# Kernel optimization log

Measured on AMD Instinct MI355X. Metric: run time of the kernel, lower is better.

## Reference

```python
import jax, jax.numpy as jnp
import numpy as np
from jax.scipy.special import logsumexp


def _lstm(x, mask, Wk, Wr, b, reverse=False):
    # x: [B,T,D], mask: [B,T] bool. Keras LSTM defaults: gate order i,f,g,o,
    # sigmoid recurrent activation, tanh activation. Masked steps carry state.
    if reverse:
        x = x[:, ::-1]
        mask = mask[:, ::-1]
    B, T, _ = x.shape
    H = Wr.shape[0]
    xz = jnp.einsum('btd,dh->bth', x, Wk) + b  # [B,T,4H] input projections, done once

    def step(carry, inp):
        h, c = carry
        z_t, m = inp  # [B,4H], [B]
        z = z_t + h @ Wr
        i, f, g, o = jnp.split(z, 4, axis=-1)
        i = jax.nn.sigmoid(i)
        f = jax.nn.sigmoid(f)
        g = jnp.tanh(g)
        o = jax.nn.sigmoid(o)
        c_new = f * c + i * g
        h_new = o * jnp.tanh(c_new)
        m = m[:, None]
        h = jnp.where(m, h_new, h)
        c = jnp.where(m, c_new, c)
        return (h, c), h

    h0 = jnp.zeros((B, H), x.dtype)
    (_, _), hs = jax.lax.scan(step, (h0, h0), (xz.transpose(1, 0, 2), mask.T))
    hs = hs.transpose(1, 0, 2)  # [B,T,H]
    if reverse:
        hs = hs[:, ::-1]
    return hs


def _crf_log_likelihood(logits, tags, lengths, trans):
    # TFA crf_log_likelihood: sequence_score - log_norm (forward algorithm)
    B, T, C = logits.shape
    t_idx = jnp.arange(T)
    mask = t_idx[None, :] < lengths[:, None]  # [B,T]
    # unary score: sum_t logits[b,t,tags[b,t]] over valid t
    unary = jnp.take_along_axis(logits, tags[..., None], axis=2)[..., 0]
    unary = jnp.sum(jnp.where(mask, unary, 0.0), axis=1)
    # binary score: sum_t trans[tags[t], tags[t+1]] for t < len-1
    binary = trans[tags[:, :-1], tags[:, 1:]]  # [B,T-1]
    mask2 = t_idx[None, : T - 1] < (lengths - 1)[:, None]
    binary = jnp.sum(jnp.where(mask2, binary, 0.0), axis=1)
    # log normalizer via forward algorithm scan
    alpha0 = logits[:, 0]  # [B,C]

    def step(alpha, inp):
        logit_t, m = inp  # [B,C], [B]
        new = logsumexp(alpha[:, :, None] + trans[None], axis=1) + logit_t
        alpha = jnp.where(m[:, None], new, alpha)
        return alpha, None

    alpha, _ = jax.lax.scan(step, alpha0,
                            (logits[:, 1:].transpose(1, 0, 2), mask[:, 1:].T))
    log_norm = logsumexp(alpha, axis=1)
    return unary + binary - log_norm


def setup_inputs() -> dict:
    key = jax.random.key(0)
    ks = jax.random.split(key, 12)
    V, D, H, C, B, T = 30000, 300, 256, 9, 64, 512
    lengths = jax.random.randint(ks[0], (B,), T // 4, T + 1).astype(jnp.int32)
    valid = jnp.arange(T)[None, :] < lengths[:, None]
    inputs = (jax.random.randint(ks[1], (B, T), 1, V) * valid).astype(jnp.int32)
    targets = (jax.random.randint(ks[2], (B, T), 0, C) * valid).astype(jnp.int32)
    s = 0.05
    return {
        'inputs': inputs,
        'inputs_length': lengths,
        'targets': targets,
        'embedding': jax.random.normal(ks[3], (V, D), jnp.float32) * s,
        'Wk_f': jax.random.normal(ks[4], (D, 4 * H), jnp.float32) * s,
        'Wr_f': jax.random.normal(ks[5], (H, 4 * H), jnp.float32) * s,
        'b_f': jnp.zeros((4 * H,), jnp.float32),
        'Wk_b': jax.random.normal(ks[6], (D, 4 * H), jnp.float32) * s,
        'Wr_b': jax.random.normal(ks[7], (H, 4 * H), jnp.float32) * s,
        'b_b': jnp.zeros((4 * H,), jnp.float32),
        'dense_W': jax.random.normal(ks[8], (2 * H, C), jnp.float32) * s,
        'dense_b': jnp.zeros((C,), jnp.float32),
        'trans': jax.random.uniform(ks[9], (C, C), jnp.float32),
    }


def reference(inputs, inputs_length, targets, embedding, Wk_f, Wr_f, b_f,
              Wk_b, Wr_b, b_b, dense_W, dense_b, trans):
    T = inputs.shape[1]
    mask = jnp.arange(T)[None, :] < inputs_length[:, None]  # [B,T]
    emb = embedding[inputs]  # [B,T,D] (dropout is identity in inference)
    h_f = _lstm(emb, mask, Wk_f, Wr_f, b_f, reverse=False)
    h_b = _lstm(emb, mask, Wk_b, Wr_b, b_b, reverse=True)
    h = jnp.concatenate([h_f, h_b], axis=-1)  # [B,T,2H]
    logits = h @ dense_W + dense_b  # [B,T,C]
    log_likelihood = _crf_log_likelihood(logits, targets, inputs_length, trans)
    return logits, log_likelihood, trans
```

## Files before the change

kernel.cpp:

```cpp
#include <hip/hip_runtime.h>
#include <cstdint>
#include <cstddef>

typedef unsigned int  u32;
typedef unsigned short u16;
typedef _Float16 f16;
typedef _Float16 f16x2 __attribute__((ext_vector_type(2)));
typedef _Float16 half8 __attribute__((ext_vector_type(8)));
typedef float    f32x4v __attribute__((ext_vector_type(4)));
typedef int      i32x4 __attribute__((ext_vector_type(4)));

#define BATCH 64
#define TSEQ  512
#define DEMB  300
#define KPAD  320
#define HDIM  256
#define G4    1024
#define NCLS  9

__device__ __forceinline__ u32 packf16(float a, float b) {
  f16x2 v; v.x = (f16)a; v.y = (f16)b;
  return __builtin_bit_cast(u32, v);
}
__device__ __forceinline__ float f16f(u16 x) {
  return (float)__builtin_bit_cast(f16, x);
}
__device__ __forceinline__ float sigm_fast(float x) {
  return __builtin_amdgcn_rcpf(1.f + __expf(-x));
}
__device__ __forceinline__ float tanh_fast(float x) {
  float ax = __builtin_fabsf(x);
  float e = __expf(-2.f * ax);
  float t = (1.f - e) * __builtin_amdgcn_rcpf(1.f + e);
  return copysignf(t, x);
}

__global__ __launch_bounds__(256) void embcvt_k(const float* __restrict__ emb,
                                                u16* __restrict__ out) {
  const int v  = blockIdx.x * 16 + (threadIdx.x >> 4);
  const int kc = threadIdx.x & 15;
  u32* __restrict__ dst = (u32*)(out + (size_t)v * KPAD + kc * 20);
  if (kc < 15) {
    const float* __restrict__ src = emb + (size_t)v * DEMB + kc * 20;
    float tmp[20];
#pragma unroll
    for (int j = 0; j < 20; ++j) tmp[j] = src[j];
#pragma unroll
    for (int j = 0; j < 10; ++j) dst[j] = packf16(tmp[2 * j], tmp[2 * j + 1]);
  } else {
#pragma unroll
    for (int j = 0; j < 10; ++j) dst[j] = 0u;
  }
}

__global__ __launch_bounds__(256) void wkt_k(const float* __restrict__ Wk_f,
                                             const float* __restrict__ Wk_b,
                                             u16* __restrict__ wkt) {
  const int dir = blockIdx.y;
  const float* __restrict__ Wk = dir ? Wk_b : Wk_f;
  const int col = blockIdx.x * 16 + (threadIdx.x >> 4);
  const int kc  = threadIdx.x & 15;
  u32* __restrict__ dst = (u32*)(wkt + ((size_t)dir * G4 + col) * KPAD + kc * 20);
  if (kc < 15) {
    float tmp[20];
#pragma unroll
    for (int j = 0; j < 20; ++j) tmp[j] = Wk[(size_t)(kc * 20 + j) * G4 + col];
#pragma unroll
    for (int j = 0; j < 10; ++j) dst[j] = packf16(tmp[2 * j], tmp[2 * j + 1]);
  } else {
#pragma unroll
    for (int j = 0; j < 10; ++j) dst[j] = 0u;
  }
}

__global__ __launch_bounds__(256) void wr8_k(const float* __restrict__ Wr_f,
                                             const float* __restrict__ Wr_b,
                                             signed char* __restrict__ wr8) {
  const int dir = blockIdx.y;
  const float* __restrict__ Wr = dir ? Wr_b : Wr_f;
  const int col = blockIdx.x * 16 + (threadIdx.x >> 4);
  const int k0  = (threadIdx.x & 15) * 16;
  float tmp[16];
#pragma unroll
  for (int j = 0; j < 16; ++j) tmp[j] = Wr[(size_t)(k0 + j) * G4 + col];
  u32 pw[4];
#pragma unroll
  for (int jj = 0; jj < 4; ++jj) {
    u32 p = 0;
#pragma unroll
    for (int b = 0; b < 4; ++b) {
      int q = (int)__builtin_rintf(tmp[4 * jj + b] * 512.f);
      q = q > 127 ? 127 : (q < -127 ? -127 : q);
      p |= ((u32)(q & 255)) << (8 * b);
    }
    pw[jj] = p;
  }
  *(uint4*)(wr8 + ((size_t)dir * G4 + col) * HDIM + k0) =
      make_uint4(pw[0], pw[1], pw[2], pw[3]);
}

__global__ __launch_bounds__(256) void xz_gemm_k(
    const int* __restrict__ inputs, const u16* __restrict__ wkt,
    const u16* __restrict__ embf16, const float* __restrict__ b_f,
    const float* __restrict__ b_b, u16* __restrict__ xz)
{
  __shared__ __align__(16) u16 As[128 * 40];
  __shared__ __align__(16) u16 Bs[128 * 40];
  const int tid  = threadIdx.x;
  const int wv   = tid >> 6, lane = tid & 63;
  const int quad = lane >> 4, fl = lane & 15;
  const int cbi  = blockIdx.x;
  const int dir  = cbi >> 3;
  const int cb1  = (cbi & 7) * 128;
  const int rb   = blockIdx.y * 128;
  const float* __restrict__ bias = dir ? b_b : b_f;

  const int sm = tid >> 1, sh = (tid & 1) * 16;
  const int vrow = inputs[rb + sm];
  const u16* __restrict__ asrc = wkt + ((size_t)(dir * G4) + cb1 + sm) * KPAD + sh;
  const u16* __restrict__ bsrc = embf16 + (size_t)vrow * KPAD + sh;

  f32x4v acc[2][8];
#pragma unroll
  for (int bt = 0; bt < 2; ++bt)
#pragma unroll
    for (int i = 0; i < 8; ++i) acc[bt][i] = (f32x4v){0.f, 0.f, 0.f, 0.f};

  for (int kt = 0; kt < 10; ++kt) {
    const int k0 = kt * 32;
    uint4 a0v = *(const uint4*)(asrc + k0);
    uint4 a1v = *(const uint4*)(asrc + k0 + 8);
    uint4 b0v = *(const uint4*)(bsrc + k0);
    uint4 b1v = *(const uint4*)(bsrc + k0 + 8);
    *(uint4*)&As[sm * 40 + sh]     = a0v;
    *(uint4*)&As[sm * 40 + sh + 8] = a1v;
    *(uint4*)&Bs[sm * 40 + sh]     = b0v;
    *(uint4*)&Bs[sm * 40 + sh + 8] = b1v;
    __syncthreads();
    half8 bf[2];
#pragma unroll
    for (int bt = 0; bt < 2; ++bt)
      bf[bt] = *(const half8*)&Bs[(wv * 32 + bt * 16 + fl) * 40 + quad * 8];
#pragma unroll
    for (int i = 0; i < 8; ++i) {
      half8 af = *(const half8*)&As[(i * 16 + fl) * 40 + quad * 8];
      acc[0][i] = __builtin_amdgcn_mfma_f32_16x16x32_f16(af, bf[0], acc[0][i], 0, 0, 0);
      acc[1][i] = __builtin_amdgcn_mfma_f32_16x16x32_f16(af, bf[1], acc[1][i], 0, 0, 0);
    }
    __syncthreads();
  }
#pragma unroll
  for (int bt = 0; bt < 2; ++bt) {
    const int row = rb + wv * 32 + bt * 16 + fl;
    u16* __restrict__ orow = xz + ((size_t)(dir * BATCH * TSEQ) + row) * G4;
#pragma unroll
    for (int i = 0; i < 8; ++i) {
      const int mb = cb1 + i * 16 + quad * 4;
      const float4 bb = *(const float4*)&bias[mb];
      f32x4v v = acc[bt][i];
      uint2 pk;
      pk.x = packf16(v[0] + bb.x, v[1] + bb.y);
      pk.y = packf16(v[2] + bb.z, v[3] + bb.w);
      *(uint2*)&orow[mb] = pk;
    }
  }
}

#define MFI(a, b, c) __builtin_amdgcn_mfma_i32_16x16x64_i8(a, b, c, 0, 0, 0)
#define LD8(g, ct, kc) (*(const i32x4*)(wr8w + (size_t)((g) * 256 + 32 * w + (ct) * 16 + l15) * HDIM + (kc) * 64 + q16))
#define DECL8(g, ct) \
  i32x4 W##g##ct##_0 = LD8(g, ct, 0), W##g##ct##_1 = LD8(g, ct, 1), \
        W##g##ct##_2 = LD8(g, ct, 2), W##g##ct##_3 = LD8(g, ct, 3); \
  asm volatile("" : "+a"(W##g##ct##_0), "+a"(W##g##ct##_1), \
                    "+a"(W##g##ct##_2), "+a"(W##g##ct##_3));
#define TILE(g, ct) \
  i32x4 ac##g##ct = (i32x4){0, 0, 0, 0}; \
  ac##g##ct = MFI(af0, W##g##ct##_0, ac##g##ct); \
  ac##g##ct = MFI(af1, W##g##ct##_1, ac##g##ct); \
  ac##g##ct = MFI(af2, W##g##ct##_2, ac##g##ct); \
  ac##g##ct = MFI(af3, W##g##ct##_3, ac##g##ct);

__global__ __launch_bounds__(512, 2) void lstm_k(
    const u16* __restrict__ xz, const signed char* __restrict__ wr8,
    const int* __restrict__ lengths, u16* __restrict__ hcat)
{
  const int chain = blockIdx.x;
  const int dir   = chain >> 6;
  const int batch = chain & 63;
  const int tid  = threadIdx.x;
  const int w    = tid >> 6;
  const int lane = tid & 63;
  const int quad = lane >> 4, l15 = lane & 15;
  const int q16  = quad * 16;
  const int ctsel = quad & 1;
  const int j    = 32 * w + ctsel * 16 + l15;
  const int wr   = quad < 2;
  const float DEQ = 1.f / (512.f * 127.f);

  __shared__ __align__(16) signed char hpk[2][256];

  const signed char* __restrict__ wr8w = wr8 + (size_t)dir * G4 * HDIM;

  DECL8(0, 0) DECL8(0, 1) DECL8(1, 0) DECL8(1, 1)
  DECL8(2, 0) DECL8(2, 1) DECL8(3, 0) DECL8(3, 1)

  if (tid < 256) hpk[0][tid] = 0;

  float c = 0.f, h = 0.f;
  const int len = lengths[batch];
  const u16* __restrict__ xzb = xz + (size_t)(dir * BATCH + batch) * TSEQ * G4;
  u16* __restrict__ hrow = hcat + (size_t)batch * TSEQ * 512 + dir * 256;
  __syncthreads();

  int tt = dir ? (TSEQ - 1) : 0;
  const int dt = dir ? -1 : 1;
  u16 x0 = xzb[(size_t)tt * G4 + j];
  u16 x1 = xzb[(size_t)tt * G4 + 256 + j];
  u16 x2 = xzb[(size_t)tt * G4 + 512 + j];
  u16 x3 = xzb[(size_t)tt * G4 + 768 + j];

  for (int st = 0; st < TSEQ; ++st) {
    const int ttn = (st == TSEQ - 1) ? tt : tt + dt;
    u16 xn0 = xzb[(size_t)ttn * G4 + j];
    u16 xn1 = xzb[(size_t)ttn * G4 + 256 + j];
    u16 xn2 = xzb[(size_t)ttn * G4 + 512 + j];
    u16 xn3 = xzb[(size_t)ttn * G4 + 768 + j];

    const int par = st & 1;
    const signed char* hb = &hpk[par][0];
    i32x4 af0 = *(const i32x4*)(hb + q16);
    i32x4 af1 = *(const i32x4*)(hb + 64 + q16);
    i32x4 af2 = *(const i32x4*)(hb + 128 + q16);
    i32x4 af3 = *(const i32x4*)(hb + 192 + q16);

    TILE(0, 0) TILE(0, 1)
    TILE(1, 0) TILE(1, 1)
    TILE(2, 0) TILE(2, 1)
    TILE(3, 0) TILE(3, 1)

    int ri = ctsel ? ac01[0] : ac00[0];
    int rf = ctsel ? ac11[0] : ac10[0];
    int rg = ctsel ? ac21[0] : ac20[0];
    int ro = ctsel ? ac31[0] : ac30[0];

    float zi = (float)ri * DEQ + f16f(x0);
    float zf = (float)rf * DEQ + f16f(x1);
    float zg = (float)rg * DEQ + f16f(x2);
    float zo = (float)ro * DEQ + f16f(x3);
    float ig = sigm_fast(zi);
    float fg = sigm_fast(zf);
    float gg = tanh_fast(zg);
    float og = sigm_fast(zo);
    float cn = fg * c + ig * gg;
    float hn = og * tanh_fast(cn);
    if (tt < len) { c = cn; h = hn; }
    if (wr) {
      u32 hb2 = packf16(h, h);
      hrow[(size_t)tt * 512 + j] = (u16)(hb2 & 0xffffu);
      int hq = (int)__builtin_rintf(h * 127.f);
      hpk[par ^ 1][j] = (signed char)hq;
    }
    __syncthreads();
    x0 = xn0; x1 = xn1; x2 = xn2; x3 = xn3; tt = ttn;
  }
}

__global__ __launch_bounds__(256) void dense_k(
    const u16* __restrict__ hcat, const float* __restrict__ W,
    const float* __restrict__ bias, float* __restrict__ out)
{
  const int lane = threadIdx.x & 63;
  const int wv = threadIdx.x >> 6;
  const int rowbase = (blockIdx.x * 4 + wv) * 8;
  for (int rr = 0; rr < 8; ++rr) {
    const int row = rowbase + rr;
    const u16* __restrict__ hr = hcat + (size_t)row * 512;
    float hv[8];
#pragma unroll
    for (int i = 0; i < 8; ++i)
      hv[i] = f16f(hr[i * 64 + lane]);
    float myout = 0.f;
#pragma unroll
    for (int cc = 0; cc < 9; ++cc) {
      float p = 0.f;
#pragma unroll
      for (int i = 0; i < 8; ++i)
        p = fmaf(hv[i], W[(size_t)(i * 64 + lane) * 9 + cc], p);
#pragma unroll
      for (int o = 32; o > 0; o >>= 1) p += __shfl_xor(p, o);
      if (lane == cc) myout = p + bias[cc];
    }
    if (lane < 9) out[(size_t)row * 9 + lane] = myout;
  }
}

__global__ __launch_bounds__(64) void crf_k(
    const float* __restrict__ logits, const int* __restrict__ tags,
    const int* __restrict__ lengths, const float* __restrict__ trans,
    float* __restrict__ out_ll, float* __restrict__ out_trans)
{
  const int b = blockIdx.x;
  const int lane = threadIdx.x;
  const int len = lengths[b];
  const float* __restrict__ lg = logits + (size_t)b * TSEQ * NCLS;
  const int* __restrict__ tg = tags + (size_t)b * TSEQ;

  float ua = 0.f, ba = 0.f;
  for (int t = lane; t < TSEQ; t += 64) {
    int tag = tg[t];
    if (t < len) ua += lg[t * 9 + tag];
    if (t < len - 1) ba += trans[tag * 9 + tg[t + 1]];
  }
  float s = ua + ba;
#pragma unroll
  for (int o = 32; o > 0; o >>= 1) s += __shfl_xor(s, o);

  const int j = (lane < 9) ? lane : 0;
  float trc[9], alpha[9];
#pragma unroll
  for (int i = 0; i < 9; ++i) trc[i] = trans[i * 9 + j];
#pragma unroll
  for (int i = 0; i < 9; ++i) alpha[i] = lg[i];
  for (int t = 1; t < TSEQ; ++t) {
    if (t >= len) break;
    float m = -1e30f;
#pragma unroll
    for (int i = 0; i < 9; ++i) m = fmaxf(m, alpha[i] + trc[i]);
    float ss = 0.f;
#pragma unroll
    for (int i = 0; i < 9; ++i) ss += __expf(alpha[i] + trc[i] - m);
    float nj = __logf(ss) + m + lg[t * 9 + j];
#pragma unroll
    for (int i = 0; i < 9; ++i) alpha[i] = __shfl(nj, i);
  }
  float m2 = -1e30f;
#pragma unroll
  for (int i = 0; i < 9; ++i) m2 = fmaxf(m2, alpha[i]);
  float s2 = 0.f;
#pragma unroll
  for (int i = 0; i < 9; ++i) s2 += __expf(alpha[i] - m2);
  float lse = __logf(s2) + m2;
  if (lane == 0) out_ll[b] = s - lse;
  if (b == 0)
    for (int i = lane; i < 81; i += 64) out_trans[i] = trans[i];
}

extern "C" void kernel_launch(void* const* d_in, const int* in_sizes, int n_in,
                              void* d_out, int out_size, void* d_ws, size_t ws_size,
                              hipStream_t stream)
{
  const int*   inputs  = (const int*)d_in[0];
  const int*   lengths = (const int*)d_in[1];
  const int*   targets = (const int*)d_in[2];
  const float* emb     = (const float*)d_in[3];
  const float* Wk_f    = (const float*)d_in[4];
  const float* Wr_f    = (const float*)d_in[5];
  const float* b_f     = (const float*)d_in[6];
  const float* Wk_b    = (const float*)d_in[7];
  const float* Wr_b    = (const float*)d_in[8];
  const float* b_b     = (const float*)d_in[9];
  const float* dense_W = (const float*)d_in[10];
  const float* dense_b = (const float*)d_in[11];
  const float* trans   = (const float*)d_in[12];

  char* ws = (char*)d_ws;
  u16*         wkt    = (u16*)ws;
  signed char* wr8    = (signed char*)(ws + 1310720ull);
  u16*         embf16 = (u16*)(ws + 1835008ull);
  u16*         xz     = (u16*)(ws + 1835008ull + 19200000ull);
  u16*         hcat   = (u16*)(ws + 1835008ull + 19200000ull + 134217728ull);

  float* out_logits = (float*)d_out;
  float* out_ll     = out_logits + (size_t)BATCH * TSEQ * NCLS;
  float* out_trans  = out_ll + BATCH;

  hipLaunchKernelGGL(embcvt_k, dim3(1875), dim3(256), 0, stream, emb, embf16);
  hipLaunchKernelGGL(wkt_k, dim3(64, 2), dim3(256), 0, stream, Wk_f, Wk_b, wkt);
  hipLaunchKernelGGL(wr8_k, dim3(64, 2), dim3(256), 0, stream, Wr_f, Wr_b, wr8);
  hipLaunchKernelGGL(xz_gemm_k, dim3(16, 256), dim3(256), 0, stream,
                     inputs, wkt, embf16, b_f, b_b, xz);
  hipLaunchKernelGGL(lstm_k, dim3(128), dim3(512), 0, stream,
                     xz, wr8, lengths, hcat);
  hipLaunchKernelGGL(dense_k, dim3(1024), dim3(256), 0, stream,
                     hcat, dense_W, dense_b, out_logits);
  hipLaunchKernelGGL(crf_k, dim3(64), dim3(64), 0, stream,
                     out_logits, targets, lengths, trans, out_ll, out_trans);
}
```

Before: 718.9 us.

## Interleave gate projections, prefetch GEMM tiles, defer h stores, vectorize conversions

The xz projection buffer is stored gate-interleaved (four gates per hidden unit adjacent), so each LSTM step loads one ushort4 instead of four scattered u16 values. The xz GEMM register-prefetches the next K tile while the current one computes, the LSTM defers each hidden-state global store by one step so it overlaps the recurrent MFMAs, the embedding conversion uses float4 loads, and the CRF loop prefetches the next step's logits. The interleaved GEMM epilogue now writes scalar 16-bit values at stride 4, which may hurt store coalescing there.

```diff
diff --git a/kernel.cpp b/kernel.cpp
--- a/kernel.cpp
+++ b/kernel.cpp
@@ -39,17 +39,18 @@
                                                 u16* __restrict__ out) {
   const int v  = blockIdx.x * 16 + (threadIdx.x >> 4);
   const int kc = threadIdx.x & 15;
-  u32* __restrict__ dst = (u32*)(out + (size_t)v * KPAD + kc * 20);
+  uint2* __restrict__ dst = (uint2*)(out + (size_t)v * KPAD + kc * 20);
   if (kc < 15) {
-    const float* __restrict__ src = emb + (size_t)v * DEMB + kc * 20;
-    float tmp[20];
-#pragma unroll
-    for (int j = 0; j < 20; ++j) tmp[j] = src[j];
-#pragma unroll
-    for (int j = 0; j < 10; ++j) dst[j] = packf16(tmp[2 * j], tmp[2 * j + 1]);
+    const float4* __restrict__ s4 = (const float4*)(emb + (size_t)v * DEMB + kc * 20);
+    float4 f0 = s4[0], f1 = s4[1], f2 = s4[2], f3 = s4[3], f4 = s4[4];
+    dst[0] = make_uint2(packf16(f0.x, f0.y), packf16(f0.z, f0.w));
+    dst[1] = make_uint2(packf16(f1.x, f1.y), packf16(f1.z, f1.w));
+    dst[2] = make_uint2(packf16(f2.x, f2.y), packf16(f2.z, f2.w));
+    dst[3] = make_uint2(packf16(f3.x, f3.y), packf16(f3.z, f3.w));
+    dst[4] = make_uint2(packf16(f4.x, f4.y), packf16(f4.z, f4.w));
   } else {
 #pragma unroll
-    for (int j = 0; j < 10; ++j) dst[j] = 0u;
+    for (int j = 0; j < 5; ++j) dst[j] = make_uint2(0u, 0u);
   }
 }
 
@@ -102,7 +103,7 @@
 __global__ __launch_bounds__(256) void xz_gemm_k(
     const int* __restrict__ inputs, const u16* __restrict__ wkt,
     const u16* __restrict__ embf16, const float* __restrict__ b_f,
-    const float* __restrict__ b_b, u16* __restrict__ xz)
+    const float* __restrict__ b_b, u16* __restrict__ xzp)
 {
   __shared__ __align__(16) u16 As[128 * 40];
   __shared__ __align__(16) u16 Bs[128 * 40];
@@ -126,17 +127,24 @@
 #pragma unroll
     for (int i = 0; i < 8; ++i) acc[bt][i] = (f32x4v){0.f, 0.f, 0.f, 0.f};
 
+  uint4 a0v = *(const uint4*)(asrc);
+  uint4 a1v = *(const uint4*)(asrc + 8);
+  uint4 b0v = *(const uint4*)(bsrc);
+  uint4 b1v = *(const uint4*)(bsrc + 8);
+
   for (int kt = 0; kt < 10; ++kt) {
-    const int k0 = kt * 32;
-    uint4 a0v = *(const uint4*)(asrc + k0);
-    uint4 a1v = *(const uint4*)(asrc + k0 + 8);
-    uint4 b0v = *(const uint4*)(bsrc + k0);
-    uint4 b1v = *(const uint4*)(bsrc + k0 + 8);
     *(uint4*)&As[sm * 40 + sh]     = a0v;
     *(uint4*)&As[sm * 40 + sh + 8] = a1v;
     *(uint4*)&Bs[sm * 40 + sh]     = b0v;
     *(uint4*)&Bs[sm * 40 + sh + 8] = b1v;
     __syncthreads();
+    if (kt < 9) {
+      const int k1 = (kt + 1) * 32;
+      a0v = *(const uint4*)(asrc + k1);
+      a1v = *(const uint4*)(asrc + k1 + 8);
+      b0v = *(const uint4*)(bsrc + k1);
+      b1v = *(const uint4*)(bsrc + k1 + 8);
+    }
     half8 bf[2];
 #pragma unroll
     for (int bt = 0; bt < 2; ++bt)
@@ -152,16 +160,18 @@
 #pragma unroll
   for (int bt = 0; bt < 2; ++bt) {
     const int row = rb + wv * 32 + bt * 16 + fl;
-    u16* __restrict__ orow = xz + ((size_t)(dir * BATCH * TSEQ) + row) * G4;
+    u16* __restrict__ obase = xzp + ((size_t)(dir * BATCH * TSEQ + row) << 10);
 #pragma unroll
     for (int i = 0; i < 8; ++i) {
       const int mb = cb1 + i * 16 + quad * 4;
+      const int g = mb >> 8, jb = mb & 255;
       const float4 bb = *(const float4*)&bias[mb];
       f32x4v v = acc[bt][i];
-      uint2 pk;
-      pk.x = packf16(v[0] + bb.x, v[1] + bb.y);
-      pk.y = packf16(v[2] + bb.z, v[3] + bb.w);
-      *(uint2*)&orow[mb] = pk;
+      u16* op = obase + jb * 4 + g;
+      op[0]  = (u16)(packf16(v[0] + bb.x, 0.f) & 0xffffu);
+      op[4]  = (u16)(packf16(v[1] + bb.y, 0.f) & 0xffffu);
+      op[8]  = (u16)(packf16(v[2] + bb.z, 0.f) & 0xffffu);
+      op[12] = (u16)(packf16(v[3] + bb.w, 0.f) & 0xffffu);
     }
   }
 }
@@ -181,7 +191,7 @@
   ac##g##ct = MFI(af3, W##g##ct##_3, ac##g##ct);
 
 __global__ __launch_bounds__(512, 2) void lstm_k(
-    const u16* __restrict__ xz, const signed char* __restrict__ wr8,
+    const u16* __restrict__ xzp, const signed char* __restrict__ wr8,
     const int* __restrict__ lengths, u16* __restrict__ hcat)
 {
   const int chain = blockIdx.x;
@@ -208,23 +218,19 @@
 
   float c = 0.f, h = 0.f;
   const int len = lengths[batch];
-  const u16* __restrict__ xzb = xz + (size_t)(dir * BATCH + batch) * TSEQ * G4;
+  const u16* __restrict__ xzb = xzp + ((size_t)(dir * BATCH + batch) * TSEQ << 10);
   u16* __restrict__ hrow = hcat + (size_t)batch * TSEQ * 512 + dir * 256;
   __syncthreads();
 
   int tt = dir ? (TSEQ - 1) : 0;
   const int dt = dir ? -1 : 1;
-  u16 x0 = xzb[(size_t)tt * G4 + j];
-  u16 x1 = xzb[(size_t)tt * G4 + 256 + j];
-  u16 x2 = xzb[(size_t)tt * G4 + 512 + j];
-  u16 x3 = xzb[(size_t)tt * G4 + 768 + j];
+  ushort4 xv = *(const ushort4*)(xzb + ((size_t)tt << 10) + j * 4);
+  u16 hbits_prev = 0;
+  int  tt_prev = 0;
 
   for (int st = 0; st < TSEQ; ++st) {
     const int ttn = (st == TSEQ - 1) ? tt : tt + dt;
-    u16 xn0 = xzb[(size_t)ttn * G4 + j];
-    u16 xn1 = xzb[(size_t)ttn * G4 + 256 + j];
-    u16 xn2 = xzb[(size_t)ttn * G4 + 512 + j];
-    u16 xn3 = xzb[(size_t)ttn * G4 + 768 + j];
+    ushort4 xn = *(const ushort4*)(xzb + ((size_t)ttn << 10) + j * 4);
 
     const int par = st & 1;
     const signed char* hb = &hpk[par][0];
@@ -233,6 +239,8 @@
     i32x4 af2 = *(const i32x4*)(hb + 128 + q16);
     i32x4 af3 = *(const i32x4*)(hb + 192 + q16);
 
+    if (st > 0 && wr) hrow[(size_t)tt_prev * 512 + j] = hbits_prev;
+
     TILE(0, 0) TILE(0, 1)
     TILE(1, 0) TILE(1, 1)
     TILE(2, 0) TILE(2, 1)
@@ -243,10 +251,10 @@
     int rg = ctsel ? ac21[0] : ac20[0];
     int ro = ctsel ? ac31[0] : ac30[0];
 
-    float zi = (float)ri * DEQ + f16f(x0);
-    float zf = (float)rf * DEQ + f16f(x1);
-    float zg = (float)rg * DEQ + f16f(x2);
-    float zo = (float)ro * DEQ + f16f(x3);
+    float zi = (float)ri * DEQ + f16f(xv.x);
+    float zf = (float)rf * DEQ + f16f(xv.y);
+    float zg = (float)rg * DEQ + f16f(xv.z);
+    float zo = (float)ro * DEQ + f16f(xv.w);
     float ig = sigm_fast(zi);
     float fg = sigm_fast(zf);
     float gg = tanh_fast(zg);
@@ -254,15 +262,17 @@
     float cn = fg * c + ig * gg;
     float hn = og * tanh_fast(cn);
     if (tt < len) { c = cn; h = hn; }
+    u32 hb2 = packf16(h, h);
     if (wr) {
-      u32 hb2 = packf16(h, h);
-      hrow[(size_t)tt * 512 + j] = (u16)(hb2 & 0xffffu);
       int hq = (int)__builtin_rintf(h * 127.f);
       hpk[par ^ 1][j] = (signed char)hq;
     }
+    hbits_prev = (u16)(hb2 & 0xffffu);
+    tt_prev = tt;
     __syncthreads();
-    x0 = xn0; x1 = xn1; x2 = xn2; x3 = xn3; tt = ttn;
-  }
+    xv = xn; tt = ttn;
+  }
+  if (wr) hrow[(size_t)tt_prev * 512 + j] = hbits_prev;
 }
 
 __global__ __launch_bounds__(256) void dense_k(
@@ -321,17 +331,20 @@
   for (int i = 0; i < 9; ++i) trc[i] = trans[i * 9 + j];
 #pragma unroll
   for (int i = 0; i < 9; ++i) alpha[i] = lg[i];
+  float curn = lg[9 + j];
   for (int t = 1; t < TSEQ; ++t) {
     if (t >= len) break;
+    float nxt = (t + 1 < TSEQ) ? lg[(t + 1) * 9 + j] : 0.f;
     float m = -1e30f;
 #pragma unroll
     for (int i = 0; i < 9; ++i) m = fmaxf(m, alpha[i] + trc[i]);
     float ss = 0.f;
 #pragma unroll
     for (int i = 0; i < 9; ++i) ss += __expf(alpha[i] + trc[i] - m);
-    float nj = __logf(ss) + m + lg[t * 9 + j];
+    float nj = __logf(ss) + m + curn;
 #pragma unroll
     for (int i = 0; i < 9; ++i) alpha[i] = __shfl(nj, i);
+    curn = nxt;
   }
   float m2 = -1e30f;
 #pragma unroll
@@ -367,7 +380,7 @@
   u16*         wkt    = (u16*)ws;
   signed char* wr8    = (signed char*)(ws + 1310720ull);
   u16*         embf16 = (u16*)(ws + 1835008ull);
-  u16*         xz     = (u16*)(ws + 1835008ull + 19200000ull);
+  u16*         xzp    = (u16*)(ws + 1835008ull + 19200000ull);
   u16*         hcat   = (u16*)(ws + 1835008ull + 19200000ull + 134217728ull);
 
   float* out_logits = (float*)d_out;
@@ -378,9 +391,9 @@
   hipLaunchKernelGGL(wkt_k, dim3(64, 2), dim3(256), 0, stream, Wk_f, Wk_b, wkt);
   hipLaunchKernelGGL(wr8_k, dim3(64, 2), dim3(256), 0, stream, Wr_f, Wr_b, wr8);
   hipLaunchKernelGGL(xz_gemm_k, dim3(16, 256), dim3(256), 0, stream,
-                     inputs, wkt, embf16, b_f, b_b, xz);
+                     inputs, wkt, embf16, b_f, b_b, xzp);
   hipLaunchKernelGGL(lstm_k, dim3(128), dim3(512), 0, stream,
-                     xz, wr8, lengths, hcat);
+                     xzp, wr8, lengths, hcat);
   hipLaunchKernelGGL(dense_k, dim3(1024), dim3(256), 0, stream,
                      hcat, dense_W, dense_b, out_logits);
   hipLaunchKernelGGL(crf_k, dim3(64), dim3(64), 0, stream,
```

Result: slower. 844.1 us (+17.4%).
